# Kernel optimization log

Hardware: AMD Instinct MI355X
Metric: run time of the kernel (lower is better)

The kernel has to match this reference:

```python
import jax, jax.numpy as jnp
import numpy as np

B, T, D = 8, 4096, 768

def setup_inputs() -> dict:
    key = jax.random.key(0)
    k1, k2, k3, k4, k5, k6 = jax.random.split(key, 6)
    inputs = jax.random.normal(k1, (B, T, D), dtype=jnp.float32)
    mask = jax.random.randint(k2, (B, T), 0, 2, dtype=jnp.int32)
    s = 1.0 / np.sqrt(D)
    Wq_w = jax.random.normal(k3, (D, D), dtype=jnp.float32) * s
    Wq_b = jax.random.normal(k4, (D,), dtype=jnp.float32) * 0.02
    Wk_w = jax.random.normal(k5, (D, D), dtype=jnp.float32) * s
    Wk_b = jax.random.normal(k6, (D,), dtype=jnp.float32) * 0.02
    return {"inputs": inputs, "mask": mask, "Wq_w": Wq_w, "Wq_b": Wq_b, "Wk_w": Wk_w, "Wk_b": Wk_b}

def reference(inputs, mask, Wq_w, Wq_b, Wk_w, Wk_b):
    # Linear layers (torch: x @ W.T + b)
    query = jnp.einsum('btd,ed->bte', inputs, Wq_w) + Wq_b  # (b,t,d)
    key = jnp.einsum('btd,ed->bte', inputs, Wk_w) + Wk_b    # (b,t,d)
    d_k = query.shape[-1]
    scores = jnp.einsum('bqd,bkd->bqk', query, key) / jnp.sqrt(jnp.float32(d_k))  # (b,t,t)
    # mask.unsqueeze(1): (b,1,t) broadcast over query rows
    scores = jnp.where(mask[:, None, :] == 0, jnp.float32(-1e9), scores)
    weights = jax.nn.softmax(scores, axis=2)  # (b,t,t)
    # einsum 'btd,btt->bd' == diagonal of weights, weighted sum of inputs
    w_diag = jnp.einsum('btt->bt', weights)   # (b,t)
    outputs = jnp.einsum('btd,bt->bd', inputs, w_diag)  # (b,d)
    return outputs
```

## Files before the change

### kernel.cpp

```cpp
#include <hip/hip_runtime.h>

#define BB 8
#define TT 4096
#define DD 768
#define MM (BB*TT)

typedef _Float16 f16;
typedef _Float16 f16x8 __attribute__((ext_vector_type(8)));
typedef float f32x4 __attribute__((ext_vector_type(4)));

typedef __attribute__((address_space(1))) void void_g;
typedef __attribute__((address_space(3))) void void_l;

__device__ __forceinline__ void gload16(const void* g, void* l) {
  __builtin_amdgcn_global_load_lds((void_g*)g, (void_l*)l, 16, 0, 0);
}

__global__ void cvt2_f32_f16(const float* __restrict__ a, const float* __restrict__ b,
                             f16* __restrict__ oa, f16* __restrict__ ob, int n) {
  int i = (blockIdx.x * blockDim.x + threadIdx.x) * 8;
  if (i >= 2 * n) return;
  const float* src = (i < n) ? a : b;
  f16* dst = (i < n) ? oa : ob;
  const int j = (i < n) ? i : i - n;
  float4 x = *(const float4*)(src + j);
  float4 y = *(const float4*)(src + j + 4);
  f16x8 o;
  o[0] = (f16)x.x; o[1] = (f16)x.y; o[2] = (f16)x.z; o[3] = (f16)x.w;
  o[4] = (f16)y.x; o[5] = (f16)y.y; o[6] = (f16)y.z; o[7] = (f16)y.w;
  *(f16x8*)(dst + j) = o;
}

__global__ __launch_bounds__(256)
void compact_mask(const int* __restrict__ mask, int* __restrict__ idx,
                  int* __restrict__ nbv, float* __restrict__ wdiag) {
  __shared__ int wcnt[4];
  const int b = blockIdx.x;
  const int w = threadIdx.x >> 6, l = threadIdx.x & 63;
  const int* mb = mask + b * TT + w * 1024;
  int mv[16];
  unsigned long long bal[16];
#pragma unroll
  for (int c = 0; c < 16; ++c) {
    mv[c] = mb[c * 64 + l];
    bal[c] = __ballot(mv[c] != 0);
    if (!mv[c]) wdiag[b * TT + w * 1024 + c * 64 + l] = 0.f;
  }
  int tot = 0;
#pragma unroll
  for (int c = 0; c < 16; ++c) tot += __popcll(bal[c]);
  if (l == 0) wcnt[w] = tot;
  __syncthreads();
  int base = 0;
  for (int ww = 0; ww < w; ++ww) base += wcnt[ww];
#pragma unroll
  for (int c = 0; c < 16; ++c) {
    const int pre = __popcll(bal[c] & ((1ull << l) - 1ull));
    if (mv[c]) idx[b * TT + base + pre] = w * 1024 + c * 64 + l;
    base += __popcll(bal[c]);
  }
  if (w == 3 && l == 0) nbv[b] = base;
}

__global__ __launch_bounds__(256, 3)
void proj_qkc(const float* __restrict__ Af,
              const f16* __restrict__ Wqh, const f16* __restrict__ Wkh,
              const float* __restrict__ bq, const float* __restrict__ bk,
              const int* __restrict__ idx, const int* __restrict__ nbv,
              f16* __restrict__ Qf, f16* __restrict__ Kh,
              f16* __restrict__ Xout) {
  const int b  = blockIdx.x >> 6;
  const int m0 = (blockIdx.x & 63) * 64;
  const int nb = nbv[b];
  if (m0 >= ((nb + 63) & ~63)) return;

  __shared__ f16 As[2][64 * 32];
  __shared__ f16 Ws[2][256 * 32];
  const int isK = blockIdx.z;
  const f16* Wh = isK ? Wkh : Wqh;
  const float* bias = isK ? bk : bq;
  const int n0 = blockIdx.y * 256;
  const int t = threadIdx.x;
  const int lane = t & 63;
  const int w = t >> 6;
  const int wn = w * 64;
  const int fr = lane & 15, fq = lane >> 4;
  const int xst = ((t >> 3) & 3) << 3;
  const int xrd = ((fr >> 1) & 3) << 3;

  f32x4 acc[4][4] = {};

  const int r0 = t >> 2, cA = (t & 3) * 8;
  const int e0 = t * 8;
  const int c8 = ((t & 3) ^ ((t >> 3) & 3)) * 8;
  const f16* w0 = Wh + (size_t)(n0 + r0) * DD + c8;

  const int ja = m0 + r0;
  const int tA = idx[b * TT + (ja < nb ? ja : nb - 1)];
  const float* arow = Af + ((size_t)b * TT + tA) * DD + cA;
  f16* xrow = (Xout != nullptr) ? Xout + ((size_t)b * TT + tA) * DD + cA : nullptr;
  const bool wout = (Xout != nullptr) && (!isK) && (n0 == 0);

#define PSTAGE(bf, ks_) do { \
    const int k0_ = (ks_) * 32; \
    gload16(w0 + k0_,                      &Ws[bf][w * 512]); \
    gload16(w0 + (size_t)64  * DD + k0_,   &Ws[bf][2048 + w * 512]); \
    gload16(w0 + (size_t)128 * DD + k0_,   &Ws[bf][4096 + w * 512]); \
    gload16(w0 + (size_t)192 * DD + k0_,   &Ws[bf][6144 + w * 512]); \
    { \
      const float* g0 = arow + k0_; \
      float4 x0 = *(const float4*)g0, x1 = *(const float4*)(g0 + 4); \
      f16x8 va; \
      va[0] = (f16)x0.x; va[1] = (f16)x0.y; va[2] = (f16)x0.z; va[3] = (f16)x0.w; \
      va[4] = (f16)x1.x; va[5] = (f16)x1.y; va[6] = (f16)x1.z; va[7] = (f16)x1.w; \
      *(f16x8*)&As[bf][e0 ^ xst] = va; \
      if (wout) *(f16x8*)(xrow + k0_) = va; \
    } \
  } while (0)

  PSTAGE(0, 0);
  __syncthreads();

  for (int ks = 0; ks < 24; ++ks) {
    const int bf = ks & 1;
    if (ks + 1 < 24) PSTAGE(bf ^ 1, ks + 1);
    f16x8 a[4], bfr[4];
#pragma unroll
    for (int i = 0; i < 4; ++i)
      a[i] = *(const f16x8*)&As[bf][(((i * 16 + fr) * 32) + fq * 8) ^ xrd];
#pragma unroll
    for (int j = 0; j < 4; ++j)
      bfr[j] = *(const f16x8*)&Ws[bf][(((wn + j * 16 + fr) * 32) + fq * 8) ^ xrd];
#pragma unroll
    for (int i = 0; i < 4; ++i)
#pragma unroll
      for (int j = 0; j < 4; ++j)
        acc[i][j] = __builtin_amdgcn_mfma_f32_16x16x32_f16(a[i], bfr[j], acc[i][j], 0, 0, 0);
    __syncthreads();
  }
#undef PSTAGE

#pragma unroll
  for (int j = 0; j < 4; ++j) {
    const int col = n0 + wn + j * 16 + fr;
    const float bv = bias[col];
#pragma unroll
    for (int i = 0; i < 4; ++i) {
#pragma unroll
      for (int r = 0; r < 4; ++r) {
        const int rowc = m0 + i * 16 + fq * 4 + r;
        const f16 v = (f16)(acc[i][j][r] + bv);
        if (!isK) {
          const size_t q = (size_t)b * TT * DD +
              ((((size_t)(rowc >> 6) * 24 + (col >> 5)) * 4 + ((rowc >> 4) & 3)) * 512 +
               ((rowc & 15) + (((col >> 3) & 3) << 4)) * 8 + (col & 7));
          Qf[q] = v;
        } else {
          Kh[(size_t)b * TT * DD + (size_t)rowc * DD + col] = v;
        }
      }
    }
  }
}

__global__ __launch_bounds__(256, 3)
void attn17(const f16* __restrict__ Qf, const f16* __restrict__ K,
            const int* __restrict__ nbv, float* __restrict__ pzv,
            float* __restrict__ sdg) {
  const int bid = blockIdx.x;
  const int qs = bid / 48;
  const int rem = bid % 48;
  const int kh = rem >> 3;
  const int bb = rem & 7;
  const int nb = nbv[bb];
  if (qs * 128 >= nb) return;

  __shared__ f16 Ks[2][128 * 64];
  const int t = threadIdx.x, l = t & 63, w = t >> 6;
  const int wq = w >> 1, wk = w & 1;
  const int fr = l & 15, fq = l >> 4;
  const int q0 = qs * 128;
  const float scale = 0.036084391824351613f;
  const int nkt = (nb + 127) >> 7;
  const int q6 = nkt / 6, r6 = nkt % 6;
  const int cnt = q6 + (kh < r6 ? 1 : 0);
  const int lo  = kh * q6 + (kh < r6 ? kh : r6);
  const int P = cnt * 12;

  const f16* Kg = K + (size_t)bb * TT * DD;
  const f16* qf = Qf + (size_t)bb * TT * DD + (size_t)(qs * 2 + wq) * 49152 + (size_t)l * 8;

  const int c8 = ((t & 3) ^ ((t >> 3) & 3)) * 8;
  const f16* klo = Kg + (size_t)(t >> 2) * DD + c8;
  const f16* khi = klo + (size_t)64 * DD;

  const int sx = (fq ^ ((fr >> 1) & 3)) * 8;
  const int bbase = (wk * 64 + fr) * 32 + sx;

  f32x4 acc[4][4] = {};
  f32x4 zacc[4] = {};
  int im0 = 0, im1 = 0, im2 = 0, im3 = 0;
  f16x8 avA[4], avB[4];

#define STAGE(bf, p_) do { \
    const size_t o0 = (size_t)(lo + (p_) / 12) * 128 * DD + (size_t)(((p_) % 12) * 64); \
    gload16(klo + o0,      &Ks[bf][w * 512]); \
    gload16(khi + o0,      &Ks[bf][2048 + w * 512]); \
    gload16(klo + o0 + 32, &Ks[bf][4096 + w * 512]); \
    gload16(khi + o0 + 32, &Ks[bf][6144 + w * 512]); \
  } while (0)

#define QLOAD(dst, dc_) do { \
    const f16* qp_ = qf + (size_t)(dc_) * 2048; \
    _Pragma("unroll") \
    for (int i = 0; i < 4; ++i) (dst)[i] = *(const f16x8*)(qp_ + i * 512); \
  } while (0)

#define MFMA_ALL(av_, bufv, off_) do { \
    f16x8 bv[4]; \
    _Pragma("unroll") \
    for (int j = 0; j < 4; ++j) bv[j] = *(const f16x8*)&Ks[bufv][(off_) + bbase + j * 512]; \
    __builtin_amdgcn_s_setprio(1); \
    _Pragma("unroll") \
    for (int i = 0; i < 4; ++i) \
      _Pragma("unroll") \
      for (int j = 0; j < 4; ++j) \
        acc[i][j] = __builtin_amdgcn_mfma_f32_16x16x32_f16((av_)[i], bv[j], acc[i][j], 0, 0, 0); \
    __builtin_amdgcn_s_setprio(0); \
  } while (0)

#define KT_EPILOGUE(kt_) do { \
    const float mb0 = im0 ? 0.f : -1e30f; \
    const float mb1 = im1 ? 0.f : -1e30f; \
    const float mb2 = im2 ? 0.f : -1e30f; \
    const float mb3 = im3 ? 0.f : -1e30f; \
    const bool isdiag = ((kt_) == qs); \
    _Pragma("unroll") \
    for (int i = 0; i < 4; ++i) { \
      _Pragma("unroll") \
      for (int rg = 0; rg < 4; ++rg) { \
        float v0 = fmaf(acc[i][0][rg], scale, mb0); \
        float v1 = fmaf(acc[i][1][rg], scale, mb1); \
        float v2 = fmaf(acc[i][2][rg], scale, mb2); \
        float v3 = fmaf(acc[i][3][rg], scale, mb3); \
        if (isdiag) { \
          const int rl = wq * 64 + i * 16 + fq * 4 + rg; \
          const int cl = wk * 64 + fr; \
          if (cl      == rl) sdg[(size_t)bb * TT + q0 + rl] = v0; \
          if (cl + 16 == rl) sdg[(size_t)bb * TT + q0 + rl] = v1; \
          if (cl + 32 == rl) sdg[(size_t)bb * TT + q0 + rl] = v2; \
          if (cl + 48 == rl) sdg[(size_t)bb * TT + q0 + rl] = v3; \
        } \
        zacc[i][rg] += __expf(v0) + __expf(v1) + __expf(v2) + __expf(v3); \
      } \
    } \
    _Pragma("unroll") \
    for (int i = 0; i < 4; ++i) \
      _Pragma("unroll") \
      for (int j = 0; j < 4; ++j) acc[i][j] = (f32x4)(0.f); \
  } while (0)

  STAGE(0, 0);
  QLOAD(avA, 0);
  __syncthreads();

  for (int p = 0; p < P; ++p) {
    const int buf = p & 1;
    const int kt = lo + p / 12, c = p % 12;
    if (c == 0) {
      const int cb0 = kt * 128 + wk * 64 + fr;
      im0 = (cb0 < nb); im1 = (cb0 + 16 < nb);
      im2 = (cb0 + 32 < nb); im3 = (cb0 + 48 < nb);
    }

    QLOAD(avB, 2 * c + 1);
    if (p + 1 < P) STAGE(buf ^ 1, p + 1);
    MFMA_ALL(avA, buf, 0);

    if (p + 1 < P) QLOAD(avA, 2 * (((p + 1) % 12)));
    MFMA_ALL(avB, buf, 4096);

    if (c == 11) KT_EPILOGUE(kt);

    __syncthreads();
  }
#undef STAGE
#undef QLOAD
#undef MFMA_ALL
#undef KT_EPILOGUE

  const int slot = kh * 2 + wk;
#pragma unroll
  for (int i = 0; i < 4; ++i) {
#pragma unroll
    for (int rg = 0; rg < 4; ++rg) {
      float z = zacc[i][rg];
#pragma unroll
      for (int off = 1; off < 16; off <<= 1) z += __shfl_xor(z, off);
      if (fr == 0) {
        const int row = wq * 64 + i * 16 + fq * 4 + rg;
        pzv[(size_t)slot * MM + bb * TT + q0 + row] = z;
      }
    }
  }
}

__global__ void merge12s(const float* __restrict__ pz, const float* __restrict__ sdg,
                         const int* __restrict__ idx, const int* __restrict__ nbv,
                         float* __restrict__ wdiag, float* __restrict__ out) {
  int i = blockIdx.x * 256 + threadIdx.x;
  if (i < BB * DD) out[i] = 0.f;
  if (i >= MM) return;
  const int b = i >> 12, j = i & 4095;
  if (j >= nbv[b]) return;
  float Z = 0.f;
#pragma unroll
  for (int s = 0; s < 12; ++s) Z += pz[(size_t)s * MM + i];
  wdiag[b * TT + idx[i]] = __expf(sdg[i]) / Z;
}

__global__ __launch_bounds__(256, 3)
void proj_qk(const float* __restrict__ Af,
             const f16* __restrict__ Wqh, const f16* __restrict__ Wkh,
             const float* __restrict__ bq, const float* __restrict__ bk,
             f16* __restrict__ Qf, f16* __restrict__ Kh,
             f16* __restrict__ Xout) {
  __shared__ f16 As[2][64 * 32];
  __shared__ f16 Ws[2][256 * 32];
  const int isK = blockIdx.z;
  const f16* Wh = isK ? Wkh : Wqh;
  const float* bias = isK ? bk : bq;
  const int m0 = blockIdx.x * 64;
  const int n0 = blockIdx.y * 256;
  const int t = threadIdx.x;
  const int lane = t & 63;
  const int w = t >> 6;
  const int wn = w * 64;
  const int fr = lane & 15, fq = lane >> 4;
  const int xst = ((t >> 3) & 3) << 3;
  const int xrd = ((fr >> 1) & 3) << 3;
  f32x4 acc[4][4] = {};
  const int r0 = t >> 2, cA = (t & 3) * 8;
  const int e0 = t * 8;
  const int c8 = ((t & 3) ^ ((t >> 3) & 3)) * 8;
  const f16* w0 = Wh + (size_t)(n0 + r0) * DD + c8;
  const bool wout = (Xout != nullptr) && (!isK) && (n0 == 0);

#define PSTAGE(bf, ks_) do { \
    const int k0_ = (ks_) * 32; \
    gload16(w0 + k0_,                      &Ws[bf][w * 512]); \
    gload16(w0 + (size_t)64  * DD + k0_,   &Ws[bf][2048 + w * 512]); \
    gload16(w0 + (size_t)128 * DD + k0_,   &Ws[bf][4096 + w * 512]); \
    gload16(w0 + (size_t)192 * DD + k0_,   &Ws[bf][6144 + w * 512]); \
    { \
      const float* g0 = Af + (size_t)(m0 + r0) * DD + k0_ + cA; \
      float4 x0 = *(const float4*)g0, x1 = *(const float4*)(g0 + 4); \
      f16x8 va; \
      va[0] = (f16)x0.x; va[1] = (f16)x0.y; va[2] = (f16)x0.z; va[3] = (f16)x0.w; \
      va[4] = (f16)x1.x; va[5] = (f16)x1.y; va[6] = (f16)x1.z; va[7] = (f16)x1.w; \
      *(f16x8*)&As[bf][e0 ^ xst] = va; \
      if (wout) *(f16x8*)&Xout[(size_t)(m0 + r0) * DD + k0_ + cA] = va; \
    } \
  } while (0)

  PSTAGE(0, 0);
  __syncthreads();
  for (int ks = 0; ks < 24; ++ks) {
    const int bf = ks & 1;
    if (ks + 1 < 24) PSTAGE(bf ^ 1, ks + 1);
    f16x8 a[4], b[4];
#pragma unroll
    for (int i = 0; i < 4; ++i)
      a[i] = *(const f16x8*)&As[bf][(((i * 16 + fr) * 32) + fq * 8) ^ xrd];
#pragma unroll
    for (int j = 0; j < 4; ++j)
      b[j] = *(const f16x8*)&Ws[bf][(((wn + j * 16 + fr) * 32) + fq * 8) ^ xrd];
#pragma unroll
    for (int i = 0; i < 4; ++i)
#pragma unroll
      for (int j = 0; j < 4; ++j)
        acc[i][j] = __builtin_amdgcn_mfma_f32_16x16x32_f16(a[i], b[j], acc[i][j], 0, 0, 0);
    __syncthreads();
  }
#undef PSTAGE
#pragma unroll
  for (int j = 0; j < 4; ++j) {
    const int col = n0 + wn + j * 16 + fr;
    const float bv = bias[col];
#pragma unroll
    for (int i = 0; i < 4; ++i) {
#pragma unroll
      for (int r = 0; r < 4; ++r) {
        const int row = m0 + i * 16 + fq * 4 + r;
        const f16 v = (f16)(acc[i][j][r] + bv);
        if (!isK) {
          const size_t idxq = (((size_t)(row >> 6) * 24 + (col >> 5)) * 4 +
                              ((row >> 4) & 3)) * 512 +
                             ((row & 15) + (((col >> 3) & 3) << 4)) * 8 + (col & 7);
          Qf[idxq] = v;
        } else {
          Kh[(size_t)row * DD + col] = v;
        }
      }
    }
  }
}

__global__ __launch_bounds__(256, 3)
void attn15(const f16* __restrict__ Qf, const f16* __restrict__ K,
            const int* __restrict__ mask, float* __restrict__ pzv,
            float* __restrict__ sdg) {
  __shared__ f16 Ks[2][128 * 64];
  const int bid = blockIdx.x;
  const int qs = bid / 24;
  const int kh = (bid % 24) >> 3;
  const int bb = bid & 7;
  const int t = threadIdx.x, l = t & 63, w = t >> 6;
  const int wq = w >> 1, wk = w & 1;
  const int fr = l & 15, fq = l >> 4;
  const int q0 = qs * 128;
  const float scale = 0.036084391824351613f;
  const int lo = kh * 11;
  const int cnt = (kh < 2) ? 11 : 10;
  const int P = cnt * 12;
  const f16* Kg = K + (size_t)bb * TT * DD;
  const int grp = bb * 64 + qs * 2 + wq;
  const f16* qf = Qf + (size_t)grp * 24 * 4 * 512 + (size_t)l * 8;
  const int c8 = ((t & 3) ^ ((t >> 3) & 3)) * 8;
  const f16* klo = Kg + (size_t)(t >> 2) * DD + c8;
  const f16* khi = klo + (size_t)64 * DD;
  const int sx = (fq ^ ((fr >> 1) & 3)) * 8;
  const int bbase = (wk * 64 + fr) * 32 + sx;
  f32x4 acc[4][4] = {};
  f32x4 zacc[4] = {};
  int im0 = 1, im1 = 1, im2 = 1, im3 = 1;
  f16x8 avA[4], avB[4];

#define STAGE(bf, p_) do { \
    const size_t o0 = (size_t)(lo + (p_) / 12) * 128 * DD + (size_t)(((p_) % 12) * 64); \
    gload16(klo + o0,      &Ks[bf][w * 512]); \
    gload16(khi + o0,      &Ks[bf][2048 + w * 512]); \
    gload16(klo + o0 + 32, &Ks[bf][4096 + w * 512]); \
    gload16(khi + o0 + 32, &Ks[bf][6144 + w * 512]); \
  } while (0)
#define QLOAD(dst, dc_) do { \
    const f16* qp_ = qf + (size_t)(dc_) * 2048; \
    _Pragma("unroll") \
    for (int i = 0; i < 4; ++i) (dst)[i] = *(const f16x8*)(qp_ + i * 512); \
  } while (0)
#define MFMA_ALL(av_, bufv, off_) do { \
    f16x8 bv[4]; \
    _Pragma("unroll") \
    for (int j = 0; j < 4; ++j) bv[j] = *(const f16x8*)&Ks[bufv][(off_) + bbase + j * 512]; \
    __builtin_amdgcn_s_setprio(1); \
    _Pragma("unroll") \
    for (int i = 0; i < 4; ++i) \
      _Pragma("unroll") \
      for (int j = 0; j < 4; ++j) \
        acc[i][j] = __builtin_amdgcn_mfma_f32_16x16x32_f16((av_)[i], bv[j], acc[i][j], 0, 0, 0); \
    __builtin_amdgcn_s_setprio(0); \
  } while (0)
#define KT_EPILOGUE(kt_) do { \
    const float mb0 = im0 ? 0.f : -1e30f; \
    const float mb1 = im1 ? 0.f : -1e30f; \
    const float mb2 = im2 ? 0.f : -1e30f; \
    const float mb3 = im3 ? 0.f : -1e30f; \
    const bool isdiag = ((kt_) == qs); \
    _Pragma("unroll") \
    for (int i = 0; i < 4; ++i) { \
      _Pragma("unroll") \
      for (int rg = 0; rg < 4; ++rg) { \
        float v0 = fmaf(acc[i][0][rg], scale, mb0); \
        float v1 = fmaf(acc[i][1][rg], scale, mb1); \
        float v2 = fmaf(acc[i][2][rg], scale, mb2); \
        float v3 = fmaf(acc[i][3][rg], scale, mb3); \
        if (isdiag) { \
          const int rl = wq * 64 + i * 16 + fq * 4 + rg; \
          const int cl = wk * 64 + fr; \
          if (cl      == rl) sdg[(size_t)bb * TT + q0 + rl] = v0; \
          if (cl + 16 == rl) sdg[(size_t)bb * TT + q0 + rl] = v1; \
          if (cl + 32 == rl) sdg[(size_t)bb * TT + q0 + rl] = v2; \
          if (cl + 48 == rl) sdg[(size_t)bb * TT + q0 + rl] = v3; \
        } \
        zacc[i][rg] += __expf(v0) + __expf(v1) + __expf(v2) + __expf(v3); \
      } \
    } \
    _Pragma("unroll") \
    for (int i = 0; i < 4; ++i) \
      _Pragma("unroll") \
      for (int j = 0; j < 4; ++j) acc[i][j] = (f32x4)(0.f); \
  } while (0)

  STAGE(0, 0);
  QLOAD(avA, 0);
  __syncthreads();
  for (int p = 0; p < P; ++p) {
    const int buf = p & 1;
    const int kt = lo + p / 12, c = p % 12;
    if (c == 0) {
      const int kb = bb * TT + kt * 128 + wk * 64 + fr;
      im0 = mask[kb]; im1 = mask[kb + 16]; im2 = mask[kb + 32]; im3 = mask[kb + 48];
    }
    QLOAD(avB, 2 * c + 1);
    if (p + 1 < P) STAGE(buf ^ 1, p + 1);
    MFMA_ALL(avA, buf, 0);
    if (p + 1 < P) QLOAD(avA, 2 * (((p + 1) % 12)));
    MFMA_ALL(avB, buf, 4096);
    if (c == 11) KT_EPILOGUE(kt);
    __syncthreads();
  }
#undef STAGE
#undef QLOAD
#undef MFMA_ALL
#undef KT_EPILOGUE
  const int slot = kh * 2 + wk;
#pragma unroll
  for (int i = 0; i < 4; ++i) {
#pragma unroll
    for (int rg = 0; rg < 4; ++rg) {
      float z = zacc[i][rg];
#pragma unroll
      for (int off = 1; off < 16; off <<= 1) z += __shfl_xor(z, off);
      if (fr == 0) {
        const int row = wq * 64 + i * 16 + fq * 4 + rg;
        pzv[(size_t)slot * MM + bb * TT + q0 + row] = z;
      }
    }
  }
}

__global__ void merge6(const float* __restrict__ pz, const float* __restrict__ sdg,
                       float* __restrict__ wdiag, float* __restrict__ out) {
  int i = blockIdx.x * 256 + threadIdx.x;
  if (i < BB * DD) out[i] = 0.f;
  if (i >= MM) return;
  float Z = 0.f;
#pragma unroll
  for (int s = 0; s < 6; ++s) Z += pz[(size_t)s * MM + i];
  wdiag[i] = __expf(sdg[i]) / Z;
}

__global__ __launch_bounds__(256)
void out_gemv(const float* __restrict__ X, const float* __restrict__ wdiag,
              float* __restrict__ out) {
  __shared__ float wsm[256];
  const int b = blockIdx.z;
  const int d = blockIdx.y * 256 + threadIdx.x;
  const int tbase = blockIdx.x * 256;
  wsm[threadIdx.x] = wdiag[b * TT + tbase + threadIdx.x];
  __syncthreads();
  float acc = 0.f;
  const float* xp = X + (size_t)(b * TT + tbase) * DD + d;
#pragma unroll 4
  for (int i = 0; i < 256; ++i) acc += xp[(size_t)i * DD] * wsm[i];
  atomicAdd(&out[b * DD + d], acc);
}

__global__ __launch_bounds__(256)
void out_gemv_h(const f16* __restrict__ Xh, const float* __restrict__ wdiag,
                float* __restrict__ out) {
  __shared__ float wsm[256];
  const int b = blockIdx.z;
  const int d = blockIdx.y * 256 + threadIdx.x;
  const int tbase = blockIdx.x * 256;
  wsm[threadIdx.x] = wdiag[b * TT + tbase + threadIdx.x];
  __syncthreads();
  float acc = 0.f;
  const f16* xp = Xh + (size_t)(b * TT + tbase) * DD + d;
#pragma unroll 4
  for (int i = 0; i < 256; ++i) acc += (float)xp[(size_t)i * DD] * wsm[i];
  atomicAdd(&out[b * DD + d], acc);
}

extern "C" void kernel_launch(void* const* d_in, const int* in_sizes, int n_in,
                              void* d_out, int out_size, void* d_ws, size_t ws_size,
                              hipStream_t stream) {
  const float* X    = (const float*)d_in[0];
  const int*   mask = (const int*)d_in[1];
  const float* Wq_w = (const float*)d_in[2];
  const float* Wq_b = (const float*)d_in[3];
  const float* Wk_w = (const float*)d_in[4];
  const float* Wk_b = (const float*)d_in[5];
  float* out = (float*)d_out;

  const size_t n2 = (size_t)MM * DD;
  const size_t wde = (size_t)DD * DD;

  char* p = (char*)d_ws;
  f16* Qf = (f16*)p;            p += n2 * sizeof(f16);
  f16* Kh = (f16*)p;            p += n2 * sizeof(f16);
  f16* Wqh = (f16*)p;           p += wde * sizeof(f16);
  f16* Wkh = (f16*)p;           p += wde * sizeof(f16);
  int* idx = (int*)p;           p += (size_t)MM * sizeof(int);
  int* nbv = (int*)p;           p += 64;
  float* pz = (float*)p;        p += (size_t)12 * MM * sizeof(float);
  float* sdg = (float*)p;       p += (size_t)MM * sizeof(float);
  float* wdiag = (float*)p;     p += (size_t)MM * sizeof(float);
  const size_t need_base = (size_t)(p - (char*)d_ws);
  f16* Xh = (f16*)p;
  const bool useNew = ws_size >= need_base;
  const bool useXh = ws_size >= need_base + n2 * sizeof(f16);

  if (useNew) {
    compact_mask<<<8, 256, 0, stream>>>(mask, idx, nbv, wdiag);
    cvt2_f32_f16<<<576, 256, 0, stream>>>(Wq_w, Wk_w, Wqh, Wkh, DD * DD);
    proj_qkc<<<dim3(512, 3, 2), 256, 0, stream>>>(X, Wqh, Wkh, Wq_b, Wk_b,
                                                  idx, nbv, Qf, Kh,
                                                  useXh ? Xh : (f16*)nullptr);
    attn17<<<1536, 256, 0, stream>>>(Qf, Kh, nbv, pz, sdg);
    merge12s<<<128, 256, 0, stream>>>(pz, sdg, idx, nbv, wdiag, out);
    if (useXh)
      out_gemv_h<<<dim3(16, 3, 8), 256, 0, stream>>>(Xh, wdiag, out);
    else
      out_gemv<<<dim3(16, 3, 8), 256, 0, stream>>>(X, wdiag, out);
  } else {
    f16* Qf2 = (f16*)d_ws;
    f16* Kh2 = Qf2 + n2;
    f16* Wqh2 = Kh2 + n2;
    f16* Wkh2 = Wqh2 + wde;
    float* pz2 = (float*)Wqh2;
    float* sdg2 = pz2 + 6 * (size_t)MM;
    float* wdiag2 = sdg2 + MM;
    cvt2_f32_f16<<<576, 256, 0, stream>>>(Wq_w, Wk_w, Wqh2, Wkh2, DD * DD);
    proj_qk<<<dim3(512, 3, 2), 256, 0, stream>>>(X, Wqh2, Wkh2, Wq_b, Wk_b,
                                                 Qf2, Kh2, (f16*)nullptr);
    attn15<<<768, 256, 0, stream>>>(Qf2, Kh2, mask, pz2, sdg2);
    merge6<<<128, 256, 0, stream>>>(pz2, sdg2, wdiag2, out);
    out_gemv<<<dim3(16, 3, 8), 256, 0, stream>>>(X, wdiag2, out);
  }
}
```

Baseline: 241.7 us.

## Pre-gather compacted fp16 rows and deepen projection GEMM pipeline

A new gather_cvt kernel compacts the unmasked rows of X into a contiguous fp16 buffer. The projection GEMM then loads A tiles with direct global-to-LDS loads and a 4-slot, 2-ahead prefetch using explicit waitcnt, barriers and setprio, replacing per-stage fp32 loads, conversion and an indexed gather. The output GEMV now reads the compacted fp16 rows and skips masked positions, so the wdiag scatter and zero-fill go away. The cost is one extra kernel pass and buffer, and lower occupancy from the larger LDS footprint (launch bounds drop to 2).

```diff
diff --git a/kernel.cpp b/kernel.cpp
--- a/kernel.cpp
+++ b/kernel.cpp
@@ -33,7 +33,7 @@
 
 __global__ __launch_bounds__(256)
 void compact_mask(const int* __restrict__ mask, int* __restrict__ idx,
-                  int* __restrict__ nbv, float* __restrict__ wdiag) {
+                  int* __restrict__ nbv) {
   __shared__ int wcnt[4];
   const int b = blockIdx.x;
   const int w = threadIdx.x >> 6, l = threadIdx.x & 63;
@@ -44,7 +44,6 @@
   for (int c = 0; c < 16; ++c) {
     mv[c] = mb[c * 64 + l];
     bal[c] = __ballot(mv[c] != 0);
-    if (!mv[c]) wdiag[b * TT + w * 1024 + c * 64 + l] = 0.f;
   }
   int tot = 0;
 #pragma unroll
@@ -62,20 +61,39 @@
   if (w == 3 && l == 0) nbv[b] = base;
 }
 
-__global__ __launch_bounds__(256, 3)
-void proj_qkc(const float* __restrict__ Af,
-              const f16* __restrict__ Wqh, const f16* __restrict__ Wkh,
-              const float* __restrict__ bq, const float* __restrict__ bk,
-              const int* __restrict__ idx, const int* __restrict__ nbv,
-              f16* __restrict__ Qf, f16* __restrict__ Kh,
-              f16* __restrict__ Xout) {
+__global__ __launch_bounds__(256)
+void gather_cvt(const float* __restrict__ X, const int* __restrict__ idx,
+                const int* __restrict__ nbv, f16* __restrict__ Xc) {
+  const int rr = blockIdx.x * 8 + (threadIdx.x >> 5);
+  const int b = rr >> 12, j = rr & 4095;
+  const int l = threadIdx.x & 31;
+  if (j >= nbv[b]) return;
+  const float* src = X + ((size_t)b * TT + idx[b * TT + j]) * DD + l * 24;
+  f16* dst = Xc + ((size_t)b * TT + j) * DD + l * 24;
+#pragma unroll
+  for (int c = 0; c < 3; ++c) {
+    float4 a = *(const float4*)(src + c * 8);
+    float4 d4 = *(const float4*)(src + c * 8 + 4);
+    f16x8 o;
+    o[0] = (f16)a.x;  o[1] = (f16)a.y;  o[2] = (f16)a.z;  o[3] = (f16)a.w;
+    o[4] = (f16)d4.x; o[5] = (f16)d4.y; o[6] = (f16)d4.z; o[7] = (f16)d4.w;
+    *(f16x8*)(dst + c * 8) = o;
+  }
+}
+
+__global__ __launch_bounds__(256, 2)
+void proj_qkc2(const f16* __restrict__ Xc,
+               const f16* __restrict__ Wqh, const f16* __restrict__ Wkh,
+               const float* __restrict__ bq, const float* __restrict__ bk,
+               const int* __restrict__ nbv,
+               f16* __restrict__ Qf, f16* __restrict__ Kc) {
   const int b  = blockIdx.x >> 6;
   const int m0 = (blockIdx.x & 63) * 64;
   const int nb = nbv[b];
   if (m0 >= ((nb + 63) & ~63)) return;
 
-  __shared__ f16 As[2][64 * 32];
-  __shared__ f16 Ws[2][256 * 32];
+  __shared__ f16 As[4][64 * 32];
+  __shared__ f16 Ws[4][256 * 32];
   const int isK = blockIdx.z;
   const f16* Wh = isK ? Wkh : Wqh;
   const float* bias = isK ? bk : bq;
@@ -85,58 +103,60 @@
   const int w = t >> 6;
   const int wn = w * 64;
   const int fr = lane & 15, fq = lane >> 4;
-  const int xst = ((t >> 3) & 3) << 3;
   const int xrd = ((fr >> 1) & 3) << 3;
 
   f32x4 acc[4][4] = {};
 
-  const int r0 = t >> 2, cA = (t & 3) * 8;
-  const int e0 = t * 8;
+  const int r0 = t >> 2;
   const int c8 = ((t & 3) ^ ((t >> 3) & 3)) * 8;
   const f16* w0 = Wh + (size_t)(n0 + r0) * DD + c8;
-
-  const int ja = m0 + r0;
-  const int tA = idx[b * TT + (ja < nb ? ja : nb - 1)];
-  const float* arow = Af + ((size_t)b * TT + tA) * DD + cA;
-  f16* xrow = (Xout != nullptr) ? Xout + ((size_t)b * TT + tA) * DD + cA : nullptr;
-  const bool wout = (Xout != nullptr) && (!isK) && (n0 == 0);
-
-#define PSTAGE(bf, ks_) do { \
+  const f16* a0 = Xc + (size_t)b * TT * DD + (size_t)(m0 + r0) * DD + c8;
+
+#define PSTAGE(sl, ks_) do { \
     const int k0_ = (ks_) * 32; \
-    gload16(w0 + k0_,                      &Ws[bf][w * 512]); \
-    gload16(w0 + (size_t)64  * DD + k0_,   &Ws[bf][2048 + w * 512]); \
-    gload16(w0 + (size_t)128 * DD + k0_,   &Ws[bf][4096 + w * 512]); \
-    gload16(w0 + (size_t)192 * DD + k0_,   &Ws[bf][6144 + w * 512]); \
-    { \
-      const float* g0 = arow + k0_; \
-      float4 x0 = *(const float4*)g0, x1 = *(const float4*)(g0 + 4); \
-      f16x8 va; \
-      va[0] = (f16)x0.x; va[1] = (f16)x0.y; va[2] = (f16)x0.z; va[3] = (f16)x0.w; \
-      va[4] = (f16)x1.x; va[5] = (f16)x1.y; va[6] = (f16)x1.z; va[7] = (f16)x1.w; \
-      *(f16x8*)&As[bf][e0 ^ xst] = va; \
-      if (wout) *(f16x8*)(xrow + k0_) = va; \
-    } \
+    gload16(a0 + k0_,                      &As[sl][w * 512]); \
+    gload16(w0 + k0_,                      &Ws[sl][w * 512]); \
+    gload16(w0 + (size_t)64  * DD + k0_,   &Ws[sl][2048 + w * 512]); \
+    gload16(w0 + (size_t)128 * DD + k0_,   &Ws[sl][4096 + w * 512]); \
+    gload16(w0 + (size_t)192 * DD + k0_,   &Ws[sl][6144 + w * 512]); \
   } while (0)
 
   PSTAGE(0, 0);
-  __syncthreads();
+  PSTAGE(1, 1);
+  asm volatile("s_waitcnt vmcnt(5)" ::: "memory");
+  __builtin_amdgcn_sched_barrier(0);
+  __builtin_amdgcn_s_barrier();
 
   for (int ks = 0; ks < 24; ++ks) {
-    const int bf = ks & 1;
-    if (ks + 1 < 24) PSTAGE(bf ^ 1, ks + 1);
+    const int sl = ks & 3;
+    if (ks + 2 < 24) {
+      PSTAGE((ks + 2) & 3, ks + 2);
+      asm volatile("s_waitcnt vmcnt(10)" ::: "memory");
+    } else if (ks + 1 < 24) {
+      asm volatile("s_waitcnt vmcnt(5)" ::: "memory");
+    } else {
+      asm volatile("s_waitcnt vmcnt(0)" ::: "memory");
+    }
+    __builtin_amdgcn_sched_barrier(0);
+    __builtin_amdgcn_s_barrier();
+    __builtin_amdgcn_sched_barrier(0);
+
     f16x8 a[4], bfr[4];
 #pragma unroll
     for (int i = 0; i < 4; ++i)
-      a[i] = *(const f16x8*)&As[bf][(((i * 16 + fr) * 32) + fq * 8) ^ xrd];
+      a[i] = *(const f16x8*)&As[sl][(((i * 16 + fr) * 32) + fq * 8) ^ xrd];
 #pragma unroll
     for (int j = 0; j < 4; ++j)
-      bfr[j] = *(const f16x8*)&Ws[bf][(((wn + j * 16 + fr) * 32) + fq * 8) ^ xrd];
+      bfr[j] = *(const f16x8*)&Ws[sl][(((wn + j * 16 + fr) * 32) + fq * 8) ^ xrd];
+    __builtin_amdgcn_s_setprio(1);
 #pragma unroll
     for (int i = 0; i < 4; ++i)
 #pragma unroll
       for (int j = 0; j < 4; ++j)
         acc[i][j] = __builtin_amdgcn_mfma_f32_16x16x32_f16(a[i], bfr[j], acc[i][j], 0, 0, 0);
-    __syncthreads();
+    __builtin_amdgcn_s_setprio(0);
+    __builtin_amdgcn_sched_barrier(0);
+    __builtin_amdgcn_s_barrier();
   }
 #undef PSTAGE
 
@@ -156,7 +176,7 @@
                ((rowc & 15) + (((col >> 3) & 3) << 4)) * 8 + (col & 7));
           Qf[q] = v;
         } else {
-          Kh[(size_t)b * TT * DD + (size_t)rowc * DD + col] = v;
+          Kc[(size_t)b * TT * DD + (size_t)rowc * DD + col] = v;
         }
       }
     }
@@ -305,26 +325,43 @@
   }
 }
 
-__global__ void merge12s(const float* __restrict__ pz, const float* __restrict__ sdg,
-                         const int* __restrict__ idx, const int* __restrict__ nbv,
-                         float* __restrict__ wdiag, float* __restrict__ out) {
+__global__ void merge12c(const float* __restrict__ pz, const float* __restrict__ sdg,
+                         const int* __restrict__ nbv,
+                         float* __restrict__ wdiagc, float* __restrict__ out) {
   int i = blockIdx.x * 256 + threadIdx.x;
   if (i < BB * DD) out[i] = 0.f;
   if (i >= MM) return;
   const int b = i >> 12, j = i & 4095;
-  if (j >= nbv[b]) return;
+  if (j >= nbv[b]) { wdiagc[i] = 0.f; return; }
   float Z = 0.f;
 #pragma unroll
   for (int s = 0; s < 12; ++s) Z += pz[(size_t)s * MM + i];
-  wdiag[b * TT + idx[i]] = __expf(sdg[i]) / Z;
+  wdiagc[i] = __expf(sdg[i]) / Z;
+}
+
+__global__ __launch_bounds__(256)
+void out_gemv_c(const f16* __restrict__ Xc, const float* __restrict__ wdiagc,
+                const int* __restrict__ nbv, float* __restrict__ out) {
+  __shared__ float wsm[256];
+  const int b = blockIdx.z;
+  const int nb = nbv[b];
+  const int tbase = blockIdx.x * 256;
+  if (tbase >= nb) return;
+  const int d = blockIdx.y * 256 + threadIdx.x;
+  wsm[threadIdx.x] = (tbase + threadIdx.x < nb) ? wdiagc[b * TT + tbase + threadIdx.x] : 0.f;
+  __syncthreads();
+  float acc = 0.f;
+  const f16* xp = Xc + (size_t)(b * TT + tbase) * DD + d;
+  const int lim = (nb - tbase < 256) ? (nb - tbase) : 256;
+  for (int i = 0; i < lim; ++i) acc += (float)xp[(size_t)i * DD] * wsm[i];
+  atomicAdd(&out[b * DD + d], acc);
 }
 
 __global__ __launch_bounds__(256, 3)
 void proj_qk(const float* __restrict__ Af,
              const f16* __restrict__ Wqh, const f16* __restrict__ Wkh,
              const float* __restrict__ bq, const float* __restrict__ bk,
-             f16* __restrict__ Qf, f16* __restrict__ Kh,
-             f16* __restrict__ Xout) {
+             f16* __restrict__ Qf, f16* __restrict__ Kh) {
   __shared__ f16 As[2][64 * 32];
   __shared__ f16 Ws[2][256 * 32];
   const int isK = blockIdx.z;
@@ -344,7 +381,6 @@
   const int e0 = t * 8;
   const int c8 = ((t & 3) ^ ((t >> 3) & 3)) * 8;
   const f16* w0 = Wh + (size_t)(n0 + r0) * DD + c8;
-  const bool wout = (Xout != nullptr) && (!isK) && (n0 == 0);
 
 #define PSTAGE(bf, ks_) do { \
     const int k0_ = (ks_) * 32; \
@@ -359,7 +395,6 @@
       va[0] = (f16)x0.x; va[1] = (f16)x0.y; va[2] = (f16)x0.z; va[3] = (f16)x0.w; \
       va[4] = (f16)x1.x; va[5] = (f16)x1.y; va[6] = (f16)x1.z; va[7] = (f16)x1.w; \
       *(f16x8*)&As[bf][e0 ^ xst] = va; \
-      if (wout) *(f16x8*)&Xout[(size_t)(m0 + r0) * DD + k0_ + cA] = va; \
     } \
   } while (0)
 
@@ -556,22 +591,6 @@
   atomicAdd(&out[b * DD + d], acc);
 }
 
-__global__ __launch_bounds__(256)
-void out_gemv_h(const f16* __restrict__ Xh, const float* __restrict__ wdiag,
-                float* __restrict__ out) {
-  __shared__ float wsm[256];
-  const int b = blockIdx.z;
-  const int d = blockIdx.y * 256 + threadIdx.x;
-  const int tbase = blockIdx.x * 256;
-  wsm[threadIdx.x] = wdiag[b * TT + tbase + threadIdx.x];
-  __syncthreads();
-  float acc = 0.f;
-  const f16* xp = Xh + (size_t)(b * TT + tbase) * DD + d;
-#pragma unroll 4
-  for (int i = 0; i < 256; ++i) acc += (float)xp[(size_t)i * DD] * wsm[i];
-  atomicAdd(&out[b * DD + d], acc);
-}
-
 extern "C" void kernel_launch(void* const* d_in, const int* in_sizes, int n_in,
                               void* d_out, int out_size, void* d_ws, size_t ws_size,
                               hipStream_t stream) {
@@ -588,31 +607,27 @@
 
   char* p = (char*)d_ws;
   f16* Qf = (f16*)p;            p += n2 * sizeof(f16);
-  f16* Kh = (f16*)p;            p += n2 * sizeof(f16);
+  f16* Kc = (f16*)p;            p += n2 * sizeof(f16);
+  f16* Xc = (f16*)p;            p += n2 * sizeof(f16);
   f16* Wqh = (f16*)p;           p += wde * sizeof(f16);
   f16* Wkh = (f16*)p;           p += wde * sizeof(f16);
   int* idx = (int*)p;           p += (size_t)MM * sizeof(int);
   int* nbv = (int*)p;           p += 64;
   float* pz = (float*)p;        p += (size_t)12 * MM * sizeof(float);
   float* sdg = (float*)p;       p += (size_t)MM * sizeof(float);
-  float* wdiag = (float*)p;     p += (size_t)MM * sizeof(float);
-  const size_t need_base = (size_t)(p - (char*)d_ws);
-  f16* Xh = (f16*)p;
-  const bool useNew = ws_size >= need_base;
-  const bool useXh = ws_size >= need_base + n2 * sizeof(f16);
+  float* wdiagc = (float*)p;    p += (size_t)MM * sizeof(float);
+  const size_t need_new = (size_t)(p - (char*)d_ws);
+  const bool useNew = ws_size >= need_new;
 
   if (useNew) {
-    compact_mask<<<8, 256, 0, stream>>>(mask, idx, nbv, wdiag);
+    compact_mask<<<8, 256, 0, stream>>>(mask, idx, nbv);
     cvt2_f32_f16<<<576, 256, 0, stream>>>(Wq_w, Wk_w, Wqh, Wkh, DD * DD);
-    proj_qkc<<<dim3(512, 3, 2), 256, 0, stream>>>(X, Wqh, Wkh, Wq_b, Wk_b,
-                                                  idx, nbv, Qf, Kh,
-                                                  useXh ? Xh : (f16*)nullptr);
-    attn17<<<1536, 256, 0, stream>>>(Qf, Kh, nbv, pz, sdg);
-    merge12s<<<128, 256, 0, stream>>>(pz, sdg, idx, nbv, wdiag, out);
-    if (useXh)
-      out_gemv_h<<<dim3(16, 3, 8), 256, 0, stream>>>(Xh, wdiag, out);
-    else
-      out_gemv<<<dim3(16, 3, 8), 256, 0, stream>>>(X, wdiag, out);
+    gather_cvt<<<4096, 256, 0, stream>>>(X, idx, nbv, Xc);
+    proj_qkc2<<<dim3(512, 3, 2), 256, 0, stream>>>(Xc, Wqh, Wkh, Wq_b, Wk_b,
+                                                   nbv, Qf, Kc);
+    attn17<<<1536, 256, 0, stream>>>(Qf, Kc, nbv, pz, sdg);
+    merge12c<<<128, 256, 0, stream>>>(pz, sdg, nbv, wdiagc, out);
+    out_gemv_c<<<dim3(16, 3, 8), 256, 0, stream>>>(Xc, wdiagc, nbv, out);
   } else {
     f16* Qf2 = (f16*)d_ws;
     f16* Kh2 = Qf2 + n2;
@@ -623,7 +638,7 @@
     float* wdiag2 = sdg2 + MM;
     cvt2_f32_f16<<<576, 256, 0, stream>>>(Wq_w, Wk_w, Wqh2, Wkh2, DD * DD);
     proj_qk<<<dim3(512, 3, 2), 256, 0, stream>>>(X, Wqh2, Wkh2, Wq_b, Wk_b,
-                                                 Qf2, Kh2, (f16*)nullptr);
+                                                 Qf2, Kh2);
     attn15<<<768, 256, 0, stream>>>(Qf2, Kh2, mask, pz2, sdg2);
     merge6<<<128, 256, 0, stream>>>(pz2, sdg2, wdiag2, out);
     out_gemv<<<dim3(16, 3, 8), 256, 0, stream>>>(X, wdiag2, out);
```

Result: slower. 258.3 us (+6.9%).
